# Performance work log

Measured on AMD Instinct MI355X. Metric: run time of the kernel, lower is better.

The kernel has to match this reference:

```python
import jax, jax.numpy as jnp
import numpy as np

B, S, HID = 2, 2048, 2048
NH, DN, DR, DV, RANK = 16, 128, 64, 128, 512
DQK = DN + DR
SCALE = DQK ** -0.5
EPS = 1e-5


def _rope(x, theta):
    # x: [..., d] with d even; theta broadcastable to [..., d//2] (angle per pair)
    x1, x2 = x[..., 0::2], x[..., 1::2]
    c, s = jnp.cos(theta), jnp.sin(theta)
    return jnp.stack([x1 * c - x2 * s, x1 * s + x2 * c], axis=-1).reshape(x.shape)


def _layernorm(x, gamma, beta):
    mu = jnp.mean(x, axis=-1, keepdims=True)
    var = jnp.var(x, axis=-1, keepdims=True)
    return (x - mu) * jax.lax.rsqrt(var + EPS) * gamma + beta


def setup_inputs() -> dict:
    key = jax.random.key(0)
    ks = jax.random.split(key, 8)
    def xavier(k, fan_in, fan_out, gain=1.0):
        lim = gain * np.sqrt(6.0 / (fan_in + fan_out))
        return jax.random.uniform(k, (fan_in, fan_out), jnp.float32, -lim, lim)
    return {
        "hidden_states": jax.random.normal(ks[0], (B, S, HID), jnp.float32),
        "freqs_cis": jax.random.uniform(ks[1], (S, DR // 2), jnp.float32) * 2.0 * np.pi,
        "Wq": xavier(ks[2], HID, NH * DQK),                      # q_proj (stored [in,out])
        "Wkv_a": xavier(ks[3], HID, RANK + DR),                  # kv_proj_a
        "kv_gamma": jnp.ones((RANK,), jnp.float32),              # kv_norm
        "kv_beta": jnp.zeros((RANK,), jnp.float32),
        "Wkv_b": xavier(ks[4], RANK, NH * (DN + DV)),            # kv_proj_b
        "Wout": xavier(ks[5], NH * DV, HID, gain=1.0 / np.sqrt(2.0)),  # out_proj
    }


def reference(hidden_states, freqs_cis, Wq, Wkv_a, kv_gamma, kv_beta, Wkv_b, Wout):
    b, s, _ = hidden_states.shape
    max_len = freqs_cis.shape[0]
    pos = jnp.arange(s) % max_len                      # [s], position_ids=None path
    theta = freqs_cis[pos]                             # [s, DR//2]

    # Q projection, split nope/rope, partial RoPE
    q = (hidden_states @ Wq).reshape(b, s, NH, DQK)
    q_nope, q_rope = q[..., :DN], q[..., DN:]
    q_rope = _rope(q_rope, theta[None, :, None, :])    # [b,s,nh,DR]

    # Low-rank KV: compressed latent + shared rope key
    kv = hidden_states @ Wkv_a                         # [b,s,RANK+DR]
    kv_c, k_rope = kv[..., :RANK], kv[..., RANK:]
    k_rope = _rope(k_rope, theta[None, :, :])          # [b,s,DR]
    kv_c = _layernorm(kv_c, kv_gamma, kv_beta)
    kvb = (kv_c @ Wkv_b).reshape(b, s, NH, DN + DV)
    k_nope, v = kvb[..., :DN], kvb[..., DN:]
    k = jnp.concatenate(
        [k_nope, jnp.broadcast_to(k_rope[:, :, None, :], (b, s, NH, DR))], axis=-1)

    q = jnp.concatenate([q_nope, q_rope], axis=-1)     # [b,s,nh,DQK]
    scores = jnp.einsum('bthd,bshd->btsh', q, k) * SCALE
    weights = jax.nn.softmax(scores.astype(jnp.float32), axis=2).astype(q.dtype)
    attn = jnp.einsum('btsh,bshd->bthd', weights, v).reshape(b, s, NH * DV)
    return attn @ Wout
```

## Files before the change

### kernel.cpp

```cpp
#include <hip/hip_runtime.h>

#define BATCH 2
#define SEQ   2048
#define HID   2048
#define NH    16
#define DN    128
#define DR    64
#define DV    128
#define RANK  512
#define DQK   192
#define NQ    (NH*DQK)
#define NQKV  3840
#define NKVB  (NH*(DN+DV))
#define NTOK  (BATCH*SEQ)
#define SCALE_F 0.07216878364870323f
#define SCALE_LOG2E 0.10411754831420211f

typedef __bf16 bf16x8 __attribute__((ext_vector_type(8)));
typedef float  f32x4  __attribute__((ext_vector_type(4)));
typedef unsigned int u32x4 __attribute__((ext_vector_type(4)));
typedef unsigned short u16;
typedef unsigned short u16x4 __attribute__((ext_vector_type(4)));

__device__ __forceinline__ float b2f(u16 h) {
    unsigned int u = ((unsigned int)h) << 16;
    float f; __builtin_memcpy(&f, &u, 4); return f;
}
__device__ __forceinline__ u16 f2b(float f) {
    unsigned int x; __builtin_memcpy(&x, &f, 4);
    unsigned int r = x + 0x7fffu + ((x >> 16) & 1u);
    return (u16)(r >> 16);
}
__device__ __forceinline__ bf16x8 lds_frag(const u16* p) {
    u32x4 v = *(const u32x4*)p;
    return __builtin_bit_cast(bf16x8, v);
}
__device__ __forceinline__ bf16x8 to_frag(u32x4 v) {
    return __builtin_bit_cast(bf16x8, v);
}
__device__ __forceinline__ f32x4 mfma16(bf16x8 a, bf16x8 b, f32x4 c) {
    return __builtin_amdgcn_mfma_f32_16x16x32_bf16(a, b, c, 0, 0, 0);
}
__device__ __forceinline__ void store_out(u16* p, float v) { *p = f2b(v); }
__device__ __forceinline__ void store_out(float* p, float v) { *p = v; }
__device__ __forceinline__ void gld_lds16(const u16* g, u16* l) {
    __builtin_amdgcn_global_load_lds(
        (const __attribute__((address_space(1))) unsigned int*)g,
        (__attribute__((address_space(3))) unsigned int*)l, 16, 0, 0);
}

__global__ __launch_bounds__(256) void prep_kernel(
        const float* __restrict__ hs_f, u16* __restrict__ hs,
        const float* __restrict__ Wq, const float* __restrict__ Wkva,
        const float* __restrict__ Wkvb, const float* __restrict__ Wout,
        u16* __restrict__ WqkvT, u16* __restrict__ WkvbT, u16* __restrict__ WoutT) {
    int tid = threadIdx.x;
    int bid = blockIdx.x;
    if (bid < 8192) {
        int i = bid * 256 + tid;
        f32x4 v = *(const f32x4*)(hs_f + (size_t)i * 4);
        u16 o[4];
        for (int k = 0; k < 4; k++) o[k] = f2b(v[k]);
        *(unsigned long long*)(hs + (size_t)i * 4) = *(unsigned long long*)o;
        return;
    }
    bid -= 8192;
    const float* in; u16* out; int R, C, tilesC;
    if (bid < 1536)      { in = Wq;   out = WqkvT;                       R = HID;  C = NQ;   tilesC = 48; }
    else if (bid < 1920) { bid -= 1536; in = Wkva; out = WqkvT + (size_t)NQ * HID; R = HID; C = 576; tilesC = 12; }
    else if (bid < 2432) { bid -= 1920; in = Wkvb; out = WkvbT;          R = RANK; C = NKVB; tilesC = 64; }
    else                 { bid -= 2432; in = Wout; out = WoutT;          R = HID;  C = HID;  tilesC = 32; }
    __shared__ unsigned int t32[64 * 65];
    int r0 = (bid / tilesC) * 64, c0 = (bid % tilesC) * 64;
    bool valid = (c0 < C);
    for (int i = 0; i < 4; i++) {
        int u = tid + i * 256;
        int rl = u >> 4, c4 = u & 15;
        f32x4 v = {0.f, 0.f, 0.f, 0.f};
        if (valid) v = *(const f32x4*)&in[(size_t)(r0 + rl) * C + c0 + c4 * 4];
        for (int j = 0; j < 4; j++)
            t32[(c4 * 4 + j) * 65 + rl] = f2b(v[j]);
    }
    __syncthreads();
    for (int i = 0; i < 2; i++) {
        int u = tid + i * 256;
        int cl = u >> 3, r8 = (u & 7) * 8;
        unsigned int w[8];
        for (int j = 0; j < 8; j++) w[j] = t32[cl * 65 + r8 + j];
        u32x4 pk;
        for (int j = 0; j < 4; j++) pk[j] = (w[2 * j] & 0xffffu) | (w[2 * j + 1] << 16);
        *(u32x4*)&out[(size_t)(c0 + cl) * R + r0 + r8] = pk;
    }
}

template <int BM, typename OutT>
__global__ __launch_bounds__(512, 2) void gemm256k(const u16* __restrict__ A,
                                                   const u16* __restrict__ Bt,
                                                   OutT* __restrict__ C,
                                                   int K, int lda, int ldb, int ldc) {
    constexpr int MH = BM / 128;
    constexpr int NHALF = MH + 2;
    __shared__ u16 lds[2 * NHALF][128 * 64];
    int tid = threadIdx.x, lane = tid & 63, w = tid >> 6;
    int wm = w >> 2, wn = w & 3;
    int g = lane >> 4, ln = lane & 15;
    int m0 = blockIdx.y * BM, n0 = blockIdx.x * 256;

    int srow = tid >> 3, schunk = tid & 7;
    int cs = schunk ^ (srow & 7);
    int sdst = tid * 8;

    auto stage = [&](int p, int ht, int t) {
        const u16* src = (ht < MH) ? A : Bt;
        int ld = (ht < MH) ? lda : ldb;
        int base = (ht < MH) ? (m0 + ht * 128) : (n0 + (ht - MH) * 128);
        u16* buf = lds[p * NHALF + ht];
        int k0 = t << 6;
        gld_lds16(&src[(size_t)(base + srow) * ld + k0 + cs * 8], &buf[sdst]);
        gld_lds16(&src[(size_t)(base + 64 + srow) * ld + k0 + cs * 8], &buf[4096 + sdst]);
    };

    int aR = ln * 64;
    int ck0 = ((g ^ (ln & 7)) << 3);
    int ck1 = (((4 + g) ^ (ln & 7)) << 3);
    int bB = (wn & 1) * 4096;
    int aBase = (BM == 256) ? 0 : wm * 4096;

    f32x4 acc[MH * 4][4] = {};
    int NT = K >> 6;

    for (int ht = 0; ht < NHALF; ht++) stage(0, ht, 0);
    __builtin_amdgcn_sched_barrier(0);
    asm volatile("s_waitcnt vmcnt(0)" ::: "memory");
    __builtin_amdgcn_sched_barrier(0);
    __builtin_amdgcn_s_barrier();

    for (int t = 0; t < NT; t++) {
        const u16* Ab = lds[(t & 1) * NHALF + ((BM == 256) ? wm : 0)];
        const u16* Bb = lds[(t & 1) * NHALF + MH + (wn >> 1)];
        int pn = (t & 1) ^ 1;
        bool pf = (t + 1 < NT);
        bf16x8 af[4][2], bf[4][2];

#pragma unroll
        for (int f = 0; f < 4; f++) {
            af[f][0] = lds_frag(&Ab[aBase + f * 1024 + aR + ck0]);
            af[f][1] = lds_frag(&Ab[aBase + f * 1024 + aR + ck1]);
        }
#pragma unroll
        for (int nf = 0; nf < 2; nf++) {
            bf[nf][0] = lds_frag(&Bb[bB + nf * 1024 + aR + ck0]);
            bf[nf][1] = lds_frag(&Bb[bB + nf * 1024 + aR + ck1]);
        }
        if (pf) { stage(pn, 0, t + 1); stage(pn, 1, t + 1); }
        __builtin_amdgcn_s_barrier();
        __builtin_amdgcn_s_setprio(1);
#pragma unroll
        for (int f = 0; f < 4; f++)
#pragma unroll
            for (int nf = 0; nf < 2; nf++) {
                acc[f][nf] = mfma16(af[f][0], bf[nf][0], acc[f][nf]);
                acc[f][nf] = mfma16(af[f][1], bf[nf][1], acc[f][nf]);
            }
        __builtin_amdgcn_s_setprio(0);

#pragma unroll
        for (int nf = 2; nf < 4; nf++) {
            bf[nf][0] = lds_frag(&Bb[bB + nf * 1024 + aR + ck0]);
            bf[nf][1] = lds_frag(&Bb[bB + nf * 1024 + aR + ck1]);
        }
        if (pf) { for (int ht = 2; ht < NHALF; ht++) stage(pn, ht, t + 1); }
        __builtin_amdgcn_s_barrier();
        __builtin_amdgcn_s_setprio(1);
#pragma unroll
        for (int f = 0; f < 4; f++)
#pragma unroll
            for (int nf = 2; nf < 4; nf++) {
                acc[f][nf] = mfma16(af[f][0], bf[nf][0], acc[f][nf]);
                acc[f][nf] = mfma16(af[f][1], bf[nf][1], acc[f][nf]);
            }
        __builtin_amdgcn_s_setprio(0);

        if constexpr (BM == 256) {
#pragma unroll
            for (int f = 0; f < 4; f++) {
                af[f][0] = lds_frag(&Ab[(f + 4) * 1024 + aR + ck0]);
                af[f][1] = lds_frag(&Ab[(f + 4) * 1024 + aR + ck1]);
            }
            __builtin_amdgcn_s_barrier();
            __builtin_amdgcn_s_setprio(1);
#pragma unroll
            for (int f = 0; f < 4; f++)
#pragma unroll
                for (int nf = 0; nf < 2; nf++) {
                    acc[f + 4][nf] = mfma16(af[f][0], bf[nf][0], acc[f + 4][nf]);
                    acc[f + 4][nf] = mfma16(af[f][1], bf[nf][1], acc[f + 4][nf]);
                }
            __builtin_amdgcn_s_setprio(0);

            __builtin_amdgcn_s_barrier();
            __builtin_amdgcn_s_setprio(1);
#pragma unroll
            for (int f = 0; f < 4; f++)
#pragma unroll
                for (int nf = 2; nf < 4; nf++) {
                    acc[f + 4][nf] = mfma16(af[f][0], bf[nf][0], acc[f + 4][nf]);
                    acc[f + 4][nf] = mfma16(af[f][1], bf[nf][1], acc[f + 4][nf]);
                }
            __builtin_amdgcn_s_setprio(0);
        }

        if (pf) {
            __builtin_amdgcn_sched_barrier(0);
            asm volatile("s_waitcnt vmcnt(0)" ::: "memory");
            __builtin_amdgcn_sched_barrier(0);
            __builtin_amdgcn_s_barrier();
        }
    }

#pragma unroll
    for (int f = 0; f < MH * 4; f++)
#pragma unroll
        for (int nf = 0; nf < 4; nf++)
#pragma unroll
            for (int r = 0; r < 4; r++) {
                int m = m0 + ((BM == 256) ? wm * 128 : wm * 64) + f * 16 + g * 4 + r;
                int n = n0 + wn * 64 + nf * 16 + ln;
                store_out(&C[(size_t)m * ldc + n], acc[f][nf][r]);
            }
}

__global__ void rope_q(u16* __restrict__ qkv, const float* __restrict__ freqs) {
    int token = blockIdx.x;
    int s = token & (SEQ - 1);
    int tid = threadIdx.x;
    for (int i = 0; i < 2; i++) {
        int idx = tid + i * 256;
        int hh = idx >> 5, p = idx & 31;
        float th = freqs[s * 32 + p];
        float c = __cosf(th), sn = __sinf(th);
        size_t off = (size_t)token * NQKV + hh * DQK + DN + 2 * p;
        float x1 = b2f(qkv[off]), x2 = b2f(qkv[off + 1]);
        qkv[off]     = f2b(x1 * c - x2 * sn);
        qkv[off + 1] = f2b(x1 * sn + x2 * c);
    }
}

__global__ void ln_kv(const u16* __restrict__ qkv, const float* __restrict__ gamma,
                      const float* __restrict__ beta, u16* __restrict__ kv_c) {
    int row = blockIdx.x, tid = threadIdx.x;
    size_t base = (size_t)row * NQKV + NQ;
    float x0 = b2f(qkv[base + tid]), x1 = b2f(qkv[base + 256 + tid]);
    float s = x0 + x1, q2 = x0 * x0 + x1 * x1;
    for (int o = 32; o > 0; o >>= 1) { s += __shfl_xor(s, o); q2 += __shfl_xor(q2, o); }
    __shared__ float sh[8];
    int lane = tid & 63, w = tid >> 6;
    if (lane == 0) { sh[w] = s; sh[4 + w] = q2; }
    __syncthreads();
    float S = sh[0] + sh[1] + sh[2] + sh[3];
    float Q2 = sh[4] + sh[5] + sh[6] + sh[7];
    float mu = S * (1.f / 512.f);
    float var = Q2 * (1.f / 512.f) - mu * mu;
    float rs = rsqrtf(var + 1e-5f);
    kv_c[(size_t)row * RANK + tid] =
        f2b((x0 - mu) * rs * gamma[tid] + beta[tid]);
    kv_c[(size_t)row * RANK + 256 + tid] =
        f2b((x1 - mu) * rs * gamma[256 + tid] + beta[256 + tid]);
}

__global__ void k_assemble(const u16* __restrict__ kvb, const u16* __restrict__ qkv,
                           const float* __restrict__ freqs, u16* __restrict__ Kf) {
    int token = blockIdx.x;
    int b = token >> 11;
    int s = token & (SEQ - 1);
    int tid = threadIdx.x;
    __shared__ u16 roped[64];
    if (tid < 32) {
        int p = tid;
        float th = freqs[s * 32 + p];
        float c = __cosf(th), sn = __sinf(th);
        float x1 = b2f(qkv[(size_t)token * NQKV + NQ + RANK + 2 * p]);
        float x2 = b2f(qkv[(size_t)token * NQKV + NQ + RANK + 2 * p + 1]);
        roped[2 * p]     = f2b(x1 * c - x2 * sn);
        roped[2 * p + 1] = f2b(x1 * sn + x2 * c);
    }
    __syncthreads();
    int kt = s >> 6, r = s & 63;
    int swr = ((r >> 1) & 3) * 8;
    {
        int hh = tid >> 4, c8 = (tid & 15) * 8;
        size_t dst = ((size_t)(b * NH + hh) * 32 + kt) * 12288
                   + (size_t)(c8 >> 5) * 2048 + r * 32 + ((c8 & 31) ^ swr);
        *(u32x4*)&Kf[dst] = *(const u32x4*)&kvb[(size_t)token * NKVB + hh * 256 + c8];
    }
    if (tid < 128) {
        int hh = tid >> 3, c8 = (tid & 7) * 8;
        size_t dst = ((size_t)(b * NH + hh) * 32 + kt) * 12288
                   + (size_t)(4 + (c8 >> 5)) * 2048 + r * 32 + ((c8 & 31) ^ swr);
        *(u32x4*)&Kf[dst] = *(u32x4*)&roped[c8];
    }
}

__global__ void v_transpose(const u16* __restrict__ kvb, u16* __restrict__ Vt) {
    __shared__ unsigned int t32[64 * 65];
    int bx = blockIdx.x;
    int st = bx * 64, dt = blockIdx.y * 64;
    int b = blockIdx.z >> 4, h = blockIdx.z & 15;
    int tid = threadIdx.x;
    for (int i = 0; i < 2; i++) {
        int u = tid + i * 256;
        int sl = u >> 3, c8 = (u & 7) * 8;
        u32x4 v = *(const u32x4*)&kvb[((size_t)(b * SEQ + st + sl) * NH + h) * 256 + DN + dt + c8];
        for (int j = 0; j < 4; j++) {
            t32[(c8 + 2 * j) * 65 + sl]     = v[j] & 0xffffu;
            t32[(c8 + 2 * j + 1) * 65 + sl] = v[j] >> 16;
        }
    }
    __syncthreads();
    for (int i = 0; i < 2; i++) {
        int u = tid + i * 256;
        int dl = u >> 3, s8 = (u & 7) * 8;
        unsigned int w[8];
        for (int j = 0; j < 8; j++) w[j] = t32[dl * 65 + s8 + j];
        u32x4 pk;
        for (int j = 0; j < 4; j++) pk[j] = (w[2 * j] & 0xffffu) | (w[2 * j + 1] << 16);
        size_t dst = ((size_t)(b * NH + h) * 32 + bx) * 8192
                   + (size_t)(s8 >> 5) * 4096 + (size_t)(dt + dl) * 32 + (s8 & 31);
        *(u32x4*)&Vt[dst] = pk;
    }
}

#define KC    64
#define QTILE 64
#define NIT  (SEQ / KC)
__global__ __launch_bounds__(256, 3) void attn_kernel(const u16* __restrict__ Q,
                                                      const u16* __restrict__ Kf,
                                                      const u16* __restrict__ Vt,
                                                      u16* __restrict__ O) {
    __shared__ u16 Ks[6 * 64 * 32];
    __shared__ u16 Ps[QTILE * 64];
    __shared__ float lsumLDS[2][QTILE];
    int tid = threadIdx.x, lane = tid & 63, w = tid >> 6;
    int w1 = w & 1;
    int w2 = w >> 1;
    int g = lane >> 4, ln = lane & 15;
    int bid = blockIdx.x;
    int swz = ((bid & 7) << 7) | (bid >> 3);
    int qt = swz & 31, h = (swz >> 5) & 15, b = swz >> 9;

    size_t qbase = ((size_t)(b * SEQ + qt * QTILE)) * NQKV + h * DQK;
    const u16* Kh = Kf + (size_t)(b * NH + h) * (32 * 12288);
    const u16* Vh = Vt + (size_t)(b * NH + h) * (32 * 8192);

    u32x4 qreg[2][6];
#pragma unroll
    for (int ni = 0; ni < 2; ni++)
#pragma unroll
        for (int kk = 0; kk < 6; kk++) {
            const u16* qp = &Q[qbase + (size_t)(w1 * 32 + ni * 16 + ln) * NQKV + kk * 32 + g * 8];
            asm volatile("global_load_dwordx4 %0, %1, off"
                         : "=v"(qreg[ni][kk]) : "v"(qp));
        }
    const u16* kTn = Kh;
#pragma unroll
    for (int i = 0; i < 6; i++)
        gld_lds16(&kTn[i * 2048 + tid * 8], &Ks[i * 2048 + tid * 8]);

    int kRd0 = (w2 * 32 + ln) * 64 + ((g * 16) ^ (((ln >> 1) & 3) << 4));
    int kRd1 = kRd0 + 16 * 64;
    int vrow = w2 * 2048 + ln * 32 + g * 8;
    const u16* vpA = Vh + vrow;
    const u16* vpB = vpA + 4096;
    int pswz = (ln & 7) << 4;

    f32x4 oacc[2][4] = {};
    float lpriv[2] = {0.f, 0.f};

    for (int kt = 0; kt < NIT; kt++) {
        asm volatile("s_waitcnt vmcnt(0)" ::: "memory");
        __builtin_amdgcn_sched_barrier(0);
        __builtin_amdgcn_s_barrier();
        u32x4 v00, v01, v02, v03, v10, v11, v12, v13;
        asm volatile("global_load_dwordx4 %0, %1, off"             : "=v"(v00) : "v"(vpA));
        asm volatile("global_load_dwordx4 %0, %1, off offset:1024" : "=v"(v01) : "v"(vpA));
        asm volatile("global_load_dwordx4 %0, %1, off offset:2048" : "=v"(v02) : "v"(vpA));
        asm volatile("global_load_dwordx4 %0, %1, off offset:3072" : "=v"(v03) : "v"(vpA));
        asm volatile("global_load_dwordx4 %0, %1, off"             : "=v"(v10) : "v"(vpB));
        asm volatile("global_load_dwordx4 %0, %1, off offset:1024" : "=v"(v11) : "v"(vpB));
        asm volatile("global_load_dwordx4 %0, %1, off offset:2048" : "=v"(v12) : "v"(vpB));
        asm volatile("global_load_dwordx4 %0, %1, off offset:3072" : "=v"(v13) : "v"(vpB));
        const char* KsB = (const char*)Ks;
        f32x4 sacc[2][2] = {};
#pragma unroll
        for (int kk = 0; kk < 6; kk++) {
            bf16x8 af0 = lds_frag((const u16*)(KsB + kk * 4096 + kRd0));
            bf16x8 af1 = lds_frag((const u16*)(KsB + kk * 4096 + kRd1));
            bf16x8 q0 = to_frag(qreg[0][kk]), q1 = to_frag(qreg[1][kk]);
            sacc[0][0] = mfma16(af0, q0, sacc[0][0]);
            sacc[0][1] = mfma16(af0, q1, sacc[0][1]);
            sacc[1][0] = mfma16(af1, q0, sacc[1][0]);
            sacc[1][1] = mfma16(af1, q1, sacc[1][1]);
        }
        char* Pb = (char*)Ps;
#pragma unroll
        for (int mi = 0; mi < 2; mi++)
#pragma unroll
            for (int ni = 0; ni < 2; ni++) {
                float p0 = exp2f(sacc[mi][ni][0] * SCALE_LOG2E);
                float p1 = exp2f(sacc[mi][ni][1] * SCALE_LOG2E);
                float p2 = exp2f(sacc[mi][ni][2] * SCALE_LOG2E);
                float p3 = exp2f(sacc[mi][ni][3] * SCALE_LOG2E);
                lpriv[ni] += (p0 + p1) + (p2 + p3);
                unsigned int c0, c1;
                asm("v_cvt_pk_bf16_f32 %0, %1, %2" : "=v"(c0) : "v"(p0), "v"(p1));
                asm("v_cvt_pk_bf16_f32 %0, %1, %2" : "=v"(c1) : "v"(p2), "v"(p3));
                uint2 pk; pk.x = c0; pk.y = c1;
                int pwB = (w1 * 32 + ni * 16 + ln) * 128
                        + ((w2 * 64 + mi * 32 + g * 8) ^ pswz);
                *(uint2*)(Pb + pwB) = pk;
            }
        asm volatile("s_waitcnt lgkmcnt(0)" ::: "memory");
        __builtin_amdgcn_sched_barrier(0);
        __builtin_amdgcn_s_barrier();
        if (kt + 1 < NIT) {
            kTn += 12288;
#pragma unroll
            for (int i = 0; i < 6; i++)
                gld_lds16(&kTn[i * 2048 + tid * 8], &Ks[i * 2048 + tid * 8]);
            asm volatile("s_waitcnt vmcnt(6)" ::: "memory");
        } else {
            asm volatile("s_waitcnt vmcnt(0)" ::: "memory");
        }
        __builtin_amdgcn_sched_barrier(0);
        {
            bf16x8 pa0k0 = lds_frag((const u16*)(Pb + (w1 * 32 + ln) * 128 + ((g * 16) ^ pswz)));
            bf16x8 pa1k0 = lds_frag((const u16*)(Pb + (w1 * 32 + 16 + ln) * 128 + ((g * 16) ^ pswz)));
            bf16x8 pa0k1 = lds_frag((const u16*)(Pb + (w1 * 32 + ln) * 128 + ((64 + g * 16) ^ pswz)));
            bf16x8 pa1k1 = lds_frag((const u16*)(Pb + (w1 * 32 + 16 + ln) * 128 + ((64 + g * 16) ^ pswz)));
            oacc[0][0] = mfma16(pa0k0, to_frag(v00), oacc[0][0]);
            oacc[0][1] = mfma16(pa0k0, to_frag(v01), oacc[0][1]);
            oacc[0][2] = mfma16(pa0k0, to_frag(v02), oacc[0][2]);
            oacc[0][3] = mfma16(pa0k0, to_frag(v03), oacc[0][3]);
            oacc[1][0] = mfma16(pa1k0, to_frag(v00), oacc[1][0]);
            oacc[1][1] = mfma16(pa1k0, to_frag(v01), oacc[1][1]);
            oacc[1][2] = mfma16(pa1k0, to_frag(v02), oacc[1][2]);
            oacc[1][3] = mfma16(pa1k0, to_frag(v03), oacc[1][3]);
            oacc[0][0] = mfma16(pa0k1, to_frag(v10), oacc[0][0]);
            oacc[0][1] = mfma16(pa0k1, to_frag(v11), oacc[0][1]);
            oacc[0][2] = mfma16(pa0k1, to_frag(v12), oacc[0][2]);
            oacc[0][3] = mfma16(pa0k1, to_frag(v13), oacc[0][3]);
            oacc[1][0] = mfma16(pa1k1, to_frag(v10), oacc[1][0]);
            oacc[1][1] = mfma16(pa1k1, to_frag(v11), oacc[1][1]);
            oacc[1][2] = mfma16(pa1k1, to_frag(v12), oacc[1][2]);
            oacc[1][3] = mfma16(pa1k1, to_frag(v13), oacc[1][3]);
        }
        vpA += 8192; vpB += 8192;
    }

    for (int ni = 0; ni < 2; ni++) {
        float v = lpriv[ni];
        v += __shfl_xor(v, 16);
        v += __shfl_xor(v, 32);
        if (g == 0) lsumLDS[w2][w1 * 32 + ni * 16 + ln] = v;
    }
    __syncthreads();
    for (int mi = 0; mi < 2; mi++)
        for (int ni = 0; ni < 4; ni++) {
            int d = w2 * 64 + ni * 16 + ln;
            for (int r = 0; r < 4; r++) {
                int row = w1 * 32 + mi * 16 + g * 4 + r;
                float l = lsumLDS[0][row] + lsumLDS[1][row];
                O[((size_t)(b * SEQ + qt * QTILE + row) * NH + h) * DV + d] =
                    f2b(oacc[mi][ni][r] / l);
            }
        }
}

extern "C" void kernel_launch(void* const* d_in, const int* in_sizes, int n_in,
                              void* d_out, int out_size, void* d_ws, size_t ws_size,
                              hipStream_t stream) {
    const float* hs_f  = (const float*)d_in[0];
    const float* freqs = (const float*)d_in[1];
    const float* Wq    = (const float*)d_in[2];
    const float* Wkva  = (const float*)d_in[3];
    const float* gamma = (const float*)d_in[4];
    const float* beta  = (const float*)d_in[5];
    const float* Wkvb  = (const float*)d_in[6];
    const float* Wout  = (const float*)d_in[7];
    float* outp = (float*)d_out;

    char* ws = (char*)d_ws;
    size_t off = 0;
    auto alloc = [&](size_t elems) -> u16* {
        u16* p = (u16*)(ws + off);
        off += ((elems * 2 + 255) / 256) * 256;
        return p;
    };
    u16* hs     = alloc((size_t)NTOK * HID);
    u16* WqkvT  = alloc((size_t)NQKV * HID);
    u16* WkvbT  = alloc((size_t)NKVB * RANK);
    u16* WoutT  = alloc((size_t)HID * HID);
    u16* qkv    = alloc((size_t)NTOK * NQKV);
    u16* kv_c   = alloc((size_t)NTOK * RANK);
    u16* kvb    = alloc((size_t)NTOK * NKVB);
    u16* Kf     = alloc((size_t)NTOK * NQ);
    u16* Vt     = alloc((size_t)BATCH * NH * DV * SEQ);
    u16* attn   = alloc((size_t)NTOK * NH * DV);
    (void)ws_size; (void)in_sizes; (void)n_in; (void)out_size;

    prep_kernel<<<8192 + 1536 + 384 + 512 + 1024, 256, 0, stream>>>(
        hs_f, hs, Wq, Wkva, Wkvb, Wout, WqkvT, WkvbT, WoutT);

    gemm256k<256><<<dim3(NQKV / 256, NTOK / 256), 512, 0, stream>>>(hs, WqkvT, qkv, HID, HID, HID, NQKV);

    rope_q<<<NTOK, 256, 0, stream>>>(qkv, freqs);

    ln_kv<<<NTOK, 256, 0, stream>>>(qkv, gamma, beta, kv_c);

    gemm256k<256><<<dim3(NKVB / 256, NTOK / 256), 512, 0, stream>>>(kv_c, WkvbT, kvb, RANK, RANK, RANK, NKVB);

    k_assemble<<<NTOK, 256, 0, stream>>>(kvb, qkv, freqs, Kf);

    v_transpose<<<dim3(SEQ / 64, DV / 64, BATCH * NH), 256, 0, stream>>>(kvb, Vt);

    attn_kernel<<<1024, 256, 0, stream>>>(qkv, Kf, Vt, attn);

    gemm256k<128><<<dim3(HID / 256, NTOK / 128), 512, 0, stream>>>(attn, WoutT, outp, HID, HID, HID, HID);
}
```

Baseline: 420.0 us.

## Fuse small prep kernels and restructure attention loop with double-buffered P

Merges rope_q and ln_kv into one kernel, and k_assemble and v_transpose into one kernel, which removes two launches. In the attention kernel, V fragments are now loaded inside the PV phase instead of being prefetched at the top of each iteration. P is double-buffered in LDS, the hand-placed waitcnt/barrier pairs become __syncthreads, and launch bounds move from 3 to 4 blocks per CU. Dropping the early V prefetch puts global-load latency directly in front of the MFMAs, and the fused prep kernels do more work per block in exchange for fewer launches.

```diff
diff --git a/kernel.cpp b/kernel.cpp
--- a/kernel.cpp
+++ b/kernel.cpp
@@ -230,7 +230,9 @@
             }
 }
 
-__global__ void rope_q(u16* __restrict__ qkv, const float* __restrict__ freqs) {
+__global__ void rope_ln(u16* __restrict__ qkv, const float* __restrict__ freqs,
+                        const float* __restrict__ gamma, const float* __restrict__ beta,
+                        u16* __restrict__ kv_c) {
     int token = blockIdx.x;
     int s = token & (SEQ - 1);
     int tid = threadIdx.x;
@@ -244,69 +246,68 @@
         qkv[off]     = f2b(x1 * c - x2 * sn);
         qkv[off + 1] = f2b(x1 * sn + x2 * c);
     }
-}
-
-__global__ void ln_kv(const u16* __restrict__ qkv, const float* __restrict__ gamma,
-                      const float* __restrict__ beta, u16* __restrict__ kv_c) {
-    int row = blockIdx.x, tid = threadIdx.x;
-    size_t base = (size_t)row * NQKV + NQ;
+    size_t base = (size_t)token * NQKV + NQ;
     float x0 = b2f(qkv[base + tid]), x1 = b2f(qkv[base + 256 + tid]);
-    float s = x0 + x1, q2 = x0 * x0 + x1 * x1;
-    for (int o = 32; o > 0; o >>= 1) { s += __shfl_xor(s, o); q2 += __shfl_xor(q2, o); }
+    float sm = x0 + x1, q2 = x0 * x0 + x1 * x1;
+    for (int o = 32; o > 0; o >>= 1) { sm += __shfl_xor(sm, o); q2 += __shfl_xor(q2, o); }
     __shared__ float sh[8];
     int lane = tid & 63, w = tid >> 6;
-    if (lane == 0) { sh[w] = s; sh[4 + w] = q2; }
+    if (lane == 0) { sh[w] = sm; sh[4 + w] = q2; }
     __syncthreads();
     float S = sh[0] + sh[1] + sh[2] + sh[3];
     float Q2 = sh[4] + sh[5] + sh[6] + sh[7];
     float mu = S * (1.f / 512.f);
     float var = Q2 * (1.f / 512.f) - mu * mu;
     float rs = rsqrtf(var + 1e-5f);
-    kv_c[(size_t)row * RANK + tid] =
+    kv_c[(size_t)token * RANK + tid] =
         f2b((x0 - mu) * rs * gamma[tid] + beta[tid]);
-    kv_c[(size_t)row * RANK + 256 + tid] =
+    kv_c[(size_t)token * RANK + 256 + tid] =
         f2b((x1 - mu) * rs * gamma[256 + tid] + beta[256 + tid]);
 }
 
-__global__ void k_assemble(const u16* __restrict__ kvb, const u16* __restrict__ qkv,
-                           const float* __restrict__ freqs, u16* __restrict__ Kf) {
-    int token = blockIdx.x;
-    int b = token >> 11;
-    int s = token & (SEQ - 1);
+__global__ void kv_prep(const u16* __restrict__ kvb, const u16* __restrict__ qkv,
+                        const float* __restrict__ freqs, u16* __restrict__ Kf,
+                        u16* __restrict__ Vt) {
+    __shared__ unsigned int t32[64 * 65];
+    int bid = blockIdx.x;
     int tid = threadIdx.x;
-    __shared__ u16 roped[64];
-    if (tid < 32) {
-        int p = tid;
-        float th = freqs[s * 32 + p];
-        float c = __cosf(th), sn = __sinf(th);
-        float x1 = b2f(qkv[(size_t)token * NQKV + NQ + RANK + 2 * p]);
-        float x2 = b2f(qkv[(size_t)token * NQKV + NQ + RANK + 2 * p + 1]);
-        roped[2 * p]     = f2b(x1 * c - x2 * sn);
-        roped[2 * p + 1] = f2b(x1 * sn + x2 * c);
-    }
-    __syncthreads();
-    int kt = s >> 6, r = s & 63;
-    int swr = ((r >> 1) & 3) * 8;
-    {
-        int hh = tid >> 4, c8 = (tid & 15) * 8;
-        size_t dst = ((size_t)(b * NH + hh) * 32 + kt) * 12288
-                   + (size_t)(c8 >> 5) * 2048 + r * 32 + ((c8 & 31) ^ swr);
-        *(u32x4*)&Kf[dst] = *(const u32x4*)&kvb[(size_t)token * NKVB + hh * 256 + c8];
-    }
-    if (tid < 128) {
-        int hh = tid >> 3, c8 = (tid & 7) * 8;
-        size_t dst = ((size_t)(b * NH + hh) * 32 + kt) * 12288
-                   + (size_t)(4 + (c8 >> 5)) * 2048 + r * 32 + ((c8 & 31) ^ swr);
-        *(u32x4*)&Kf[dst] = *(u32x4*)&roped[c8];
-    }
-}
-
-__global__ void v_transpose(const u16* __restrict__ kvb, u16* __restrict__ Vt) {
-    __shared__ unsigned int t32[64 * 65];
-    int bx = blockIdx.x;
-    int st = bx * 64, dt = blockIdx.y * 64;
-    int b = blockIdx.z >> 4, h = blockIdx.z & 15;
-    int tid = threadIdx.x;
+    if (bid < NTOK) {
+        int token = bid;
+        int b = token >> 11;
+        int s = token & (SEQ - 1);
+        u16* roped = (u16*)t32;
+        if (tid < 32) {
+            int p = tid;
+            float th = freqs[s * 32 + p];
+            float c = __cosf(th), sn = __sinf(th);
+            float x1 = b2f(qkv[(size_t)token * NQKV + NQ + RANK + 2 * p]);
+            float x2 = b2f(qkv[(size_t)token * NQKV + NQ + RANK + 2 * p + 1]);
+            roped[2 * p]     = f2b(x1 * c - x2 * sn);
+            roped[2 * p + 1] = f2b(x1 * sn + x2 * c);
+        }
+        __syncthreads();
+        int kt = s >> 6, r = s & 63;
+        int swr = ((r >> 1) & 3) * 8;
+        {
+            int hh = tid >> 4, c8 = (tid & 15) * 8;
+            size_t dst = ((size_t)(b * NH + hh) * 32 + kt) * 12288
+                       + (size_t)(c8 >> 5) * 2048 + r * 32 + ((c8 & 31) ^ swr);
+            *(u32x4*)&Kf[dst] = *(const u32x4*)&kvb[(size_t)token * NKVB + hh * 256 + c8];
+        }
+        if (tid < 128) {
+            int hh = tid >> 3, c8 = (tid & 7) * 8;
+            size_t dst = ((size_t)(b * NH + hh) * 32 + kt) * 12288
+                       + (size_t)(4 + (c8 >> 5)) * 2048 + r * 32 + ((c8 & 31) ^ swr);
+            *(u32x4*)&Kf[dst] = *(u32x4*)&roped[c8];
+        }
+        return;
+    }
+    int rblk = bid - NTOK;
+    int bx = rblk & 31;
+    int by = (rblk >> 5) & 1;
+    int bz = rblk >> 6;
+    int st = bx * 64, dt = by * 64;
+    int b = bz >> 4, h = bz & 15;
     for (int i = 0; i < 2; i++) {
         int u = tid + i * 256;
         int sl = u >> 3, c8 = (u & 7) * 8;
@@ -333,13 +334,12 @@
 #define KC    64
 #define QTILE 64
 #define NIT  (SEQ / KC)
-__global__ __launch_bounds__(256, 3) void attn_kernel(const u16* __restrict__ Q,
+__global__ __launch_bounds__(256, 4) void attn_kernel(const u16* __restrict__ Q,
                                                       const u16* __restrict__ Kf,
                                                       const u16* __restrict__ Vt,
                                                       u16* __restrict__ O) {
     __shared__ u16 Ks[6 * 64 * 32];
-    __shared__ u16 Ps[QTILE * 64];
-    __shared__ float lsumLDS[2][QTILE];
+    __shared__ u16 Ps[2][QTILE * 64];
     int tid = threadIdx.x, lane = tid & 63, w = tid >> 6;
     int w1 = w & 1;
     int w2 = w >> 1;
@@ -361,16 +361,13 @@
             asm volatile("global_load_dwordx4 %0, %1, off"
                          : "=v"(qreg[ni][kk]) : "v"(qp));
         }
-    const u16* kTn = Kh;
 #pragma unroll
     for (int i = 0; i < 6; i++)
-        gld_lds16(&kTn[i * 2048 + tid * 8], &Ks[i * 2048 + tid * 8]);
+        gld_lds16(&Kh[i * 2048 + tid * 8], &Ks[i * 2048 + tid * 8]);
 
     int kRd0 = (w2 * 32 + ln) * 64 + ((g * 16) ^ (((ln >> 1) & 3) << 4));
     int kRd1 = kRd0 + 16 * 64;
     int vrow = w2 * 2048 + ln * 32 + g * 8;
-    const u16* vpA = Vh + vrow;
-    const u16* vpB = vpA + 4096;
     int pswz = (ln & 7) << 4;
 
     f32x4 oacc[2][4] = {};
@@ -379,16 +376,7 @@
     for (int kt = 0; kt < NIT; kt++) {
         asm volatile("s_waitcnt vmcnt(0)" ::: "memory");
         __builtin_amdgcn_sched_barrier(0);
-        __builtin_amdgcn_s_barrier();
-        u32x4 v00, v01, v02, v03, v10, v11, v12, v13;
-        asm volatile("global_load_dwordx4 %0, %1, off"             : "=v"(v00) : "v"(vpA));
-        asm volatile("global_load_dwordx4 %0, %1, off offset:1024" : "=v"(v01) : "v"(vpA));
-        asm volatile("global_load_dwordx4 %0, %1, off offset:2048" : "=v"(v02) : "v"(vpA));
-        asm volatile("global_load_dwordx4 %0, %1, off offset:3072" : "=v"(v03) : "v"(vpA));
-        asm volatile("global_load_dwordx4 %0, %1, off"             : "=v"(v10) : "v"(vpB));
-        asm volatile("global_load_dwordx4 %0, %1, off offset:1024" : "=v"(v11) : "v"(vpB));
-        asm volatile("global_load_dwordx4 %0, %1, off offset:2048" : "=v"(v12) : "v"(vpB));
-        asm volatile("global_load_dwordx4 %0, %1, off offset:3072" : "=v"(v13) : "v"(vpB));
+        __syncthreads();
         const char* KsB = (const char*)Ks;
         f32x4 sacc[2][2] = {};
 #pragma unroll
@@ -401,7 +389,7 @@
             sacc[1][0] = mfma16(af1, q0, sacc[1][0]);
             sacc[1][1] = mfma16(af1, q1, sacc[1][1]);
         }
-        char* Pb = (char*)Ps;
+        char* Pb = (char*)Ps[kt & 1];
 #pragma unroll
         for (int mi = 0; mi < 2; mi++)
 #pragma unroll
@@ -419,49 +407,38 @@
                         + ((w2 * 64 + mi * 32 + g * 8) ^ pswz);
                 *(uint2*)(Pb + pwB) = pk;
             }
-        asm volatile("s_waitcnt lgkmcnt(0)" ::: "memory");
-        __builtin_amdgcn_sched_barrier(0);
-        __builtin_amdgcn_s_barrier();
+        __syncthreads();
         if (kt + 1 < NIT) {
-            kTn += 12288;
+            const u16* kT = Kh + (size_t)(kt + 1) * 12288;
 #pragma unroll
             for (int i = 0; i < 6; i++)
-                gld_lds16(&kTn[i * 2048 + tid * 8], &Ks[i * 2048 + tid * 8]);
-            asm volatile("s_waitcnt vmcnt(6)" ::: "memory");
-        } else {
-            asm volatile("s_waitcnt vmcnt(0)" ::: "memory");
-        }
-        __builtin_amdgcn_sched_barrier(0);
-        {
-            bf16x8 pa0k0 = lds_frag((const u16*)(Pb + (w1 * 32 + ln) * 128 + ((g * 16) ^ pswz)));
-            bf16x8 pa1k0 = lds_frag((const u16*)(Pb + (w1 * 32 + 16 + ln) * 128 + ((g * 16) ^ pswz)));
-            bf16x8 pa0k1 = lds_frag((const u16*)(Pb + (w1 * 32 + ln) * 128 + ((64 + g * 16) ^ pswz)));
-            bf16x8 pa1k1 = lds_frag((const u16*)(Pb + (w1 * 32 + 16 + ln) * 128 + ((64 + g * 16) ^ pswz)));
-            oacc[0][0] = mfma16(pa0k0, to_frag(v00), oacc[0][0]);
-            oacc[0][1] = mfma16(pa0k0, to_frag(v01), oacc[0][1]);
-            oacc[0][2] = mfma16(pa0k0, to_frag(v02), oacc[0][2]);
-            oacc[0][3] = mfma16(pa0k0, to_frag(v03), oacc[0][3]);
-            oacc[1][0] = mfma16(pa1k0, to_frag(v00), oacc[1][0]);
-            oacc[1][1] = mfma16(pa1k0, to_frag(v01), oacc[1][1]);
-            oacc[1][2] = mfma16(pa1k0, to_frag(v02), oacc[1][2]);
-            oacc[1][3] = mfma16(pa1k0, to_frag(v03), oacc[1][3]);
-            oacc[0][0] = mfma16(pa0k1, to_frag(v10), oacc[0][0]);
-            oacc[0][1] = mfma16(pa0k1, to_frag(v11), oacc[0][1]);
-            oacc[0][2] = mfma16(pa0k1, to_frag(v12), oacc[0][2]);
-            oacc[0][3] = mfma16(pa0k1, to_frag(v13), oacc[0][3]);
-            oacc[1][0] = mfma16(pa1k1, to_frag(v10), oacc[1][0]);
-            oacc[1][1] = mfma16(pa1k1, to_frag(v11), oacc[1][1]);
-            oacc[1][2] = mfma16(pa1k1, to_frag(v12), oacc[1][2]);
-            oacc[1][3] = mfma16(pa1k1, to_frag(v13), oacc[1][3]);
-        }
-        vpA += 8192; vpB += 8192;
-    }
-
+                gld_lds16(&kT[i * 2048 + tid * 8], &Ks[i * 2048 + tid * 8]);
+        }
+        const u16* vT = Vh + (size_t)kt * 8192;
+#pragma unroll
+        for (int kk = 0; kk < 2; kk++) {
+            bf16x8 pa[2], vb[4];
+#pragma unroll
+            for (int mi = 0; mi < 2; mi++)
+                pa[mi] = lds_frag((const u16*)(Pb + (w1 * 32 + mi * 16 + ln) * 128
+                                               + ((kk * 64 + g * 16) ^ pswz)));
+#pragma unroll
+            for (int ni = 0; ni < 4; ni++)
+                vb[ni] = to_frag(*(const u32x4*)&vT[kk * 4096 + ni * 512 + vrow]);
+#pragma unroll
+            for (int mi = 0; mi < 2; mi++)
+#pragma unroll
+                for (int ni = 0; ni < 4; ni++)
+                    oacc[mi][ni] = mfma16(pa[mi], vb[ni], oacc[mi][ni]);
+        }
+    }
+
+    float* lsumF = (float*)Ps[0];
     for (int ni = 0; ni < 2; ni++) {
         float v = lpriv[ni];
         v += __shfl_xor(v, 16);
         v += __shfl_xor(v, 32);
-        if (g == 0) lsumLDS[w2][w1 * 32 + ni * 16 + ln] = v;
+        if (g == 0) lsumF[w2 * 64 + w1 * 32 + ni * 16 + ln] = v;
     }
     __syncthreads();
     for (int mi = 0; mi < 2; mi++)
@@ -469,7 +446,7 @@
             int d = w2 * 64 + ni * 16 + ln;
             for (int r = 0; r < 4; r++) {
                 int row = w1 * 32 + mi * 16 + g * 4 + r;
-                float l = lsumLDS[0][row] + lsumLDS[1][row];
+                float l = lsumF[row] + lsumF[64 + row];
                 O[((size_t)(b * SEQ + qt * QTILE + row) * NH + h) * DV + d] =
                     f2b(oacc[mi][ni][r] / l);
             }
@@ -513,15 +490,11 @@
 
     gemm256k<256><<<dim3(NQKV / 256, NTOK / 256), 512, 0, stream>>>(hs, WqkvT, qkv, HID, HID, HID, NQKV);
 
-    rope_q<<<NTOK, 256, 0, stream>>>(qkv, freqs);
-
-    ln_kv<<<NTOK, 256, 0, stream>>>(qkv, gamma, beta, kv_c);
+    rope_ln<<<NTOK, 256, 0, stream>>>(qkv, freqs, gamma, beta, kv_c);
 
     gemm256k<256><<<dim3(NKVB / 256, NTOK / 256), 512, 0, stream>>>(kv_c, WkvbT, kvb, RANK, RANK, RANK, NKVB);
 
-    k_assemble<<<NTOK, 256, 0, stream>>>(kvb, qkv, freqs, Kf);
-
-    v_transpose<<<dim3(SEQ / 64, DV / 64, BATCH * NH), 256, 0, stream>>>(kvb, Vt);
+    kv_prep<<<NTOK + 2048, 256, 0, stream>>>(kvb, qkv, freqs, Kf, Vt);
 
     attn_kernel<<<1024, 256, 0, stream>>>(qkv, Kf, Vt, attn);
 
```

After: 413.3 us. About the same (-1.6%).
